# Kernel tuning notes

Measured on AMD Instinct MI355X. Metric: run time of the kernel, lower is better.

The kernel has to match this reference:

```python
import jax, jax.numpy as jnp
import numpy as np

B, I, A_IN = 32, 32, 16     # batch, input capsules, input atoms
OD, OA = 10, 16             # output_dim (classes), output_atoms
H, W = 12, 12               # spatial grid
NUM_ROUTING = 3


def _squash(t):
    # squash over atom dim (axis=2): x/|x| * |x|^2/(1+|x|^2) = x*|x|/(1+|x|^2)
    norm = jnp.linalg.norm(t, axis=2, keepdims=True)
    return t * norm / (1.0 + norm * norm)


def setup_inputs() -> dict:
    key = jax.random.key(0)
    k1, k2 = jax.random.split(key)
    x = jax.random.normal(k1, (B, I, A_IN, H, W), dtype=jnp.float32)
    # torch weight: (I, A_IN, OD*OA, 1, 1), init N(0, 0.1)
    weight = 0.1 * jax.random.normal(k2, (I, A_IN, OD * OA), dtype=jnp.float32)
    # torch bias: (OD, OA, 1, 1), init const 0.1
    bias = jnp.full((OD, OA, 1, 1), 0.1, dtype=jnp.float32)
    return {"x": x, "weight": weight, "bias": bias}


def reference(x, weight, bias):
    # votes: sum over input atoms -> [B, I, OD*OA, H, W] -> [B, I, OD, OA, H, W]
    votes = jnp.einsum("biahw,iak->bikhw", x, weight)
    votes = votes.reshape(B, I, OD, OA, H, W)
    biases = jnp.broadcast_to(bias, (OD, OA, H, W))

    # Dynamic routing. In the original, logits carry no gradient (built from
    # .data), so intermediate iterations are fully stop-gradient.
    votes_sg = jax.lax.stop_gradient(votes)
    logits = jnp.zeros((B, I, OD, H, W), dtype=votes.dtype)
    activation = None
    for i in range(NUM_ROUTING):
        route = jax.nn.softmax(logits, axis=2)  # softmax over output_dim
        v = votes if i == NUM_ROUTING - 1 else votes_sg
        preact = jnp.einsum("bidhw,bidahw->bdahw", route, v) + biases
        activation = _squash(preact)  # [B, OD, OA, H, W]
        if i < NUM_ROUTING - 1:
            # agreement (dot over atoms) updates logits
            logits = logits + jnp.einsum(
                "bidahw,bdahw->bidhw", votes_sg, jax.lax.stop_gradient(activation)
            )
    return activation
```

## Files before the change

kernel.cpp:

```cpp
#include <hip/hip_runtime.h>
#include <math.h>

#define NB 32
#define NI 32
#define NA 16
#define NOD 10
#define NOA 16
#define NK 160
#define NHW 144
#define NROUT 3
#define NROWS (NB*NHW)
#define SVLD 168

__device__ __forceinline__ unsigned short f2bf(float f) {
    unsigned b = __builtin_bit_cast(unsigned, f);
    b += 0x7fffu + ((b >> 16) & 1u);
    return (unsigned short)(b >> 16);
}
__device__ __forceinline__ float bf_lo(unsigned d) {
    return __builtin_bit_cast(float, d << 16);
}
__device__ __forceinline__ float bf_hi(unsigned d) {
    return __builtin_bit_cast(float, d & 0xffff0000u);
}

__global__ __launch_bounds__(256)
void capsule_fused_kernel(const float* __restrict__ x,
                          const float* __restrict__ weight,
                          const float* __restrict__ bias,
                          float* __restrict__ out)
{
    __shared__ unsigned short sv[4][NI][SVLD];
    __shared__ __align__(16) float pool[2048];
    float* const srt_f  = pool;
    float* const sact_f = pool + 4 * NOD * 33;

    const int tid  = threadIdx.x;
    const int w    = tid >> 6;
    const int l    = tid & 63;
    const int b    = blockIdx.x / (NHW / 4);
    const int hw0  = (blockIdx.x % (NHW / 4)) * 4;

    {
        const float* xb = x + ((size_t)b * NI * NA) * NHW + hw0;
        for (int j = tid; j < NI * NA; j += 256) {
            const float4 v = *reinterpret_cast<const float4*>(xb + (size_t)j * NHW);
            *reinterpret_cast<float4*>(&pool[j * 4]) = v;
        }
    }
    __syncthreads();

    for (int j = tid; j < NI * 40; j += 256) {
        const int i  = j / 40;
        const int kq = j - i * 40;
        const int k0 = kq * 4;
        const float4* wp = reinterpret_cast<const float4*>(
            weight + (size_t)i * NA * NK + k0);
        float4 a0 = make_float4(0.f, 0.f, 0.f, 0.f);
        float4 a1 = make_float4(0.f, 0.f, 0.f, 0.f);
        float4 a2 = make_float4(0.f, 0.f, 0.f, 0.f);
        float4 a3 = make_float4(0.f, 0.f, 0.f, 0.f);
#pragma unroll
        for (int a = 0; a < NA; ++a) {
            const float4 w4 = wp[(size_t)a * 40];
            const float4 xa = *reinterpret_cast<const float4*>(&pool[(i * NA + a) * 4]);
            a0.x = fmaf(xa.x, w4.x, a0.x); a0.y = fmaf(xa.x, w4.y, a0.y);
            a0.z = fmaf(xa.x, w4.z, a0.z); a0.w = fmaf(xa.x, w4.w, a0.w);
            a1.x = fmaf(xa.y, w4.x, a1.x); a1.y = fmaf(xa.y, w4.y, a1.y);
            a1.z = fmaf(xa.y, w4.z, a1.z); a1.w = fmaf(xa.y, w4.w, a1.w);
            a2.x = fmaf(xa.z, w4.x, a2.x); a2.y = fmaf(xa.z, w4.y, a2.y);
            a2.z = fmaf(xa.z, w4.z, a2.z); a2.w = fmaf(xa.z, w4.w, a2.w);
            a3.x = fmaf(xa.w, w4.x, a3.x); a3.y = fmaf(xa.w, w4.y, a3.y);
            a3.z = fmaf(xa.w, w4.z, a3.z); a3.w = fmaf(xa.w, w4.w, a3.w);
        }
        *reinterpret_cast<ushort4*>(&sv[0][i][k0]) =
            make_ushort4(f2bf(a0.x), f2bf(a0.y), f2bf(a0.z), f2bf(a0.w));
        *reinterpret_cast<ushort4*>(&sv[1][i][k0]) =
            make_ushort4(f2bf(a1.x), f2bf(a1.y), f2bf(a1.z), f2bf(a1.w));
        *reinterpret_cast<ushort4*>(&sv[2][i][k0]) =
            make_ushort4(f2bf(a2.x), f2bf(a2.y), f2bf(a2.z), f2bf(a2.w));
        *reinterpret_cast<ushort4*>(&sv[3][i][k0]) =
            make_ushort4(f2bf(a3.x), f2bf(a3.y), f2bf(a3.z), f2bf(a3.w));
    }

    const float2 b0 = *reinterpret_cast<const float2*>(bias + 2 * l);
    float2 b1 = make_float2(0.f, 0.f);
    if (l < 16) b1 = *reinterpret_cast<const float2*>(bias + 128 + 2 * l);

    float lg[NOD];
#pragma unroll
    for (int od = 0; od < NOD; ++od) lg[od] = 0.f;
    const int iown = l & 31;

    __syncthreads();

    for (int it = 0; it < NROUT; ++it) {
        {
            float m = lg[0];
#pragma unroll
            for (int od = 1; od < NOD; ++od) m = fmaxf(m, lg[od]);
            float e[NOD];
            float s = 0.f;
#pragma unroll
            for (int od = 0; od < NOD; ++od) {
                e[od] = __expf(lg[od] - m);
                s += e[od];
            }
            const float inv = 1.f / s;
            if (l < 32) {
#pragma unroll
                for (int od = 0; od < NOD; ++od)
                    srt_f[(w * NOD + od) * 33 + iown] = e[od] * inv;
            }
        }
        __builtin_amdgcn_wave_barrier();

        {
            const int od0 = l >> 3;
            float a0 = b0.x, a1 = b0.y;
#pragma unroll
            for (int i = 0; i < NI; ++i) {
                const unsigned d = *reinterpret_cast<const unsigned*>(&sv[w][i][2 * l]);
                const float r = srt_f[(w * NOD + od0) * 33 + i];
                a0 = fmaf(r, bf_lo(d), a0);
                a1 = fmaf(r, bf_hi(d), a1);
            }
            float ss = a0 * a0 + a1 * a1;
            ss += __shfl_xor(ss, 1, 8);
            ss += __shfl_xor(ss, 2, 8);
            ss += __shfl_xor(ss, 4, 8);
            const float sc = sqrtf(ss) / (1.f + ss);
            *reinterpret_cast<float2*>(&sact_f[w * 164 + 2 * l]) =
                make_float2(a0 * sc, a1 * sc);

            if (l < 16) {
                const int od1 = 8 + (l >> 3);
                float c0 = b1.x, c1 = b1.y;
#pragma unroll
                for (int i = 0; i < NI; ++i) {
                    const unsigned d = *reinterpret_cast<const unsigned*>(&sv[w][i][128 + 2 * l]);
                    const float r = srt_f[(w * NOD + od1) * 33 + i];
                    c0 = fmaf(r, bf_lo(d), c0);
                    c1 = fmaf(r, bf_hi(d), c1);
                }
                float s2 = c0 * c0 + c1 * c1;
                s2 += __shfl_xor(s2, 1, 8);
                s2 += __shfl_xor(s2, 2, 8);
                s2 += __shfl_xor(s2, 4, 8);
                const float sc2 = sqrtf(s2) / (1.f + s2);
                *reinterpret_cast<float2*>(&sact_f[w * 164 + 128 + 2 * l]) =
                    make_float2(c0 * sc2, c1 * sc2);
            }
        }
        __builtin_amdgcn_wave_barrier();

        if (it < NROUT - 1) {
#pragma unroll
            for (int r = 0; r < 5; ++r) {
                const int t  = l + 64 * r;
                const int i  = t & 31;
                const int od = t >> 5;
                const uint4 d0 = *reinterpret_cast<const uint4*>(&sv[w][i][od * NOA]);
                const uint4 d1 = *reinterpret_cast<const uint4*>(&sv[w][i][od * NOA + 8]);
                const float* ap = &sact_f[w * 164 + od * NOA];
                const float4 c0 = *reinterpret_cast<const float4*>(ap + 0);
                const float4 c1 = *reinterpret_cast<const float4*>(ap + 4);
                const float4 c2 = *reinterpret_cast<const float4*>(ap + 8);
                const float4 c3 = *reinterpret_cast<const float4*>(ap + 12);
                float acc;
                acc  = bf_lo(d0.x) * c0.x;
                acc = fmaf(bf_hi(d0.x), c0.y, acc);
                acc = fmaf(bf_lo(d0.y), c0.z, acc);
                acc = fmaf(bf_hi(d0.y), c0.w, acc);
                acc = fmaf(bf_lo(d0.z), c1.x, acc);
                acc = fmaf(bf_hi(d0.z), c1.y, acc);
                acc = fmaf(bf_lo(d0.w), c1.z, acc);
                acc = fmaf(bf_hi(d0.w), c1.w, acc);
                acc = fmaf(bf_lo(d1.x), c2.x, acc);
                acc = fmaf(bf_hi(d1.x), c2.y, acc);
                acc = fmaf(bf_lo(d1.y), c2.z, acc);
                acc = fmaf(bf_hi(d1.y), c2.w, acc);
                acc = fmaf(bf_lo(d1.z), c3.x, acc);
                acc = fmaf(bf_hi(d1.z), c3.y, acc);
                acc = fmaf(bf_lo(d1.w), c3.z, acc);
                acc = fmaf(bf_hi(d1.w), c3.w, acc);
                srt_f[(w * NOD + od) * 33 + i] = acc;
            }
            __builtin_amdgcn_wave_barrier();
#pragma unroll
            for (int od = 0; od < NOD; ++od)
                lg[od] += srt_f[(w * NOD + od) * 33 + iown];
            __builtin_amdgcn_wave_barrier();
        }
    }

    __syncthreads();
    if (tid < NK) {
        const float4 v = make_float4(sact_f[0 * 164 + tid], sact_f[1 * 164 + tid],
                                     sact_f[2 * 164 + tid], sact_f[3 * 164 + tid]);
        *reinterpret_cast<float4*>(out + ((size_t)b * NK + tid) * NHW + hw0) = v;
    }
}

extern "C" void kernel_launch(void* const* d_in, const int* in_sizes, int n_in,
                              void* d_out, int out_size, void* d_ws, size_t ws_size,
                              hipStream_t stream) {
    const float* x      = (const float*)d_in[0];
    const float* weight = (const float*)d_in[1];
    const float* bias   = (const float*)d_in[2];
    float* out          = (float*)d_out;

    capsule_fused_kernel<<<NROWS / 4, 256, 0, stream>>>(x, weight, bias, out);
}
```

Measured before the change: 43.54 us.

## Add prepass converting weights to bf16 and transposing x for coalesced loads

Adds a prepass kernel that converts the weight tensor to bf16 and transposes x so each block's 4-pixel slab is contiguous. The main kernel then copies x with fully contiguous float4 loads and reads weights as packed bf16 uint4, halving weight traffic and changing the per-thread tiling to 8 outputs. This removes strided 16-byte gathers of x and fp32 weight reads, at the cost of an extra kernel launch, a round trip of x through workspace, and bf16 rounding of the weights. The original kernel remains as a fallback when the workspace is too small.

```diff
diff --git a/kernel.cpp b/kernel.cpp
--- a/kernel.cpp
+++ b/kernel.cpp
@@ -12,6 +12,9 @@
 #define NROWS (NB*NHW)
 #define SVLD 168
 
+#define XT_OFF 262144
+#define WS_NEEDED (XT_OFF + (size_t)NROWS * 512 * 4)
+
 __device__ __forceinline__ unsigned short f2bf(float f) {
     unsigned b = __builtin_bit_cast(unsigned, f);
     b += 0x7fffu + ((b >> 16) & 1u);
@@ -25,62 +28,115 @@
 }
 
 __global__ __launch_bounds__(256)
-void capsule_fused_kernel(const float* __restrict__ x,
-                          const float* __restrict__ weight,
-                          const float* __restrict__ bias,
-                          float* __restrict__ out)
+void prepass_kernel(const float* __restrict__ x,
+                    const float* __restrict__ weight,
+                    unsigned short* __restrict__ w_bf,
+                    float* __restrict__ x_t)
+{
+    int bid = blockIdx.x;
+    const int tid = threadIdx.x;
+    if (bid < 320) {
+        const int idx = bid * 256 + tid;
+        w_bf[idx] = f2bf(weight[idx]);
+        return;
+    }
+    bid -= 320;
+    const int b  = bid / 72;
+    const int r  = bid % 72;
+    const int jt = r / 9;
+    const int ht = r % 9;
+    const int j0 = jt * 64, hw0 = ht * 16;
+
+    __shared__ float tile[64][17];
+    {
+        const int hh = tid & 15;
+        const int j1 = tid >> 4;
+#pragma unroll
+        for (int s = 0; s < 4; ++s) {
+            const int jj = j1 + s * 16;
+            tile[jj][hh] = x[(size_t)b * 73728 + (size_t)(j0 + jj) * NHW + hw0 + hh];
+        }
+    }
+    __syncthreads();
+    {
+        const int jj = tid >> 2;
+        const int p  = tid & 3;
+#pragma unroll
+        for (int s = 0; s < 4; ++s) {
+            const int hwg = ht * 4 + s;
+            x_t[((size_t)b * 36 + hwg) * 2048 + (size_t)(j0 + jj) * 4 + p] =
+                tile[jj][s * 4 + p];
+        }
+    }
+}
+
+__global__ __launch_bounds__(256)
+void capsule_fused2_kernel(const float* __restrict__ x_t,
+                           const unsigned short* __restrict__ w_bf,
+                           const float* __restrict__ bias,
+                           float* __restrict__ out)
 {
     __shared__ unsigned short sv[4][NI][SVLD];
     __shared__ __align__(16) float pool[2048];
     float* const srt_f  = pool;
     float* const sact_f = pool + 4 * NOD * 33;
 
-    const int tid  = threadIdx.x;
-    const int w    = tid >> 6;
-    const int l    = tid & 63;
-    const int b    = blockIdx.x / (NHW / 4);
-    const int hw0  = (blockIdx.x % (NHW / 4)) * 4;
+    const int tid = threadIdx.x;
+    const int w   = tid >> 6;
+    const int l   = tid & 63;
+    const int b   = blockIdx.x / (NHW / 4);
+    const int hw0 = (blockIdx.x % (NHW / 4)) * 4;
 
     {
-        const float* xb = x + ((size_t)b * NI * NA) * NHW + hw0;
-        for (int j = tid; j < NI * NA; j += 256) {
-            const float4 v = *reinterpret_cast<const float4*>(xb + (size_t)j * NHW);
-            *reinterpret_cast<float4*>(&pool[j * 4]) = v;
-        }
-    }
-    __syncthreads();
-
-    for (int j = tid; j < NI * 40; j += 256) {
-        const int i  = j / 40;
-        const int kq = j - i * 40;
-        const int k0 = kq * 4;
-        const float4* wp = reinterpret_cast<const float4*>(
-            weight + (size_t)i * NA * NK + k0);
-        float4 a0 = make_float4(0.f, 0.f, 0.f, 0.f);
-        float4 a1 = make_float4(0.f, 0.f, 0.f, 0.f);
-        float4 a2 = make_float4(0.f, 0.f, 0.f, 0.f);
-        float4 a3 = make_float4(0.f, 0.f, 0.f, 0.f);
+        const float4* src = reinterpret_cast<const float4*>(x_t + (size_t)blockIdx.x * 2048);
+        float4* dst = reinterpret_cast<float4*>(pool);
+        dst[tid]       = src[tid];
+        dst[tid + 256] = src[tid + 256];
+    }
+    __syncthreads();
+
+    for (int t = tid; t < NI * 20; t += 256) {
+        const int i  = t / 20;
+        const int ko = t - i * 20;
+        const int k0 = ko * 8;
+        const uint4* wp = reinterpret_cast<const uint4*>(w_bf + (size_t)i * NA * NK + k0);
+        float4 acc[4][2];
+#pragma unroll
+        for (int p = 0; p < 4; ++p) {
+            acc[p][0] = make_float4(0.f, 0.f, 0.f, 0.f);
+            acc[p][1] = make_float4(0.f, 0.f, 0.f, 0.f);
+        }
 #pragma unroll
         for (int a = 0; a < NA; ++a) {
-            const float4 w4 = wp[(size_t)a * 40];
+            const uint4 wv = wp[(size_t)a * 20];
+            const float w0 = bf_lo(wv.x), w1 = bf_hi(wv.x);
+            const float w2 = bf_lo(wv.y), w3 = bf_hi(wv.y);
+            const float w4 = bf_lo(wv.z), w5 = bf_hi(wv.z);
+            const float w6 = bf_lo(wv.w), w7 = bf_hi(wv.w);
             const float4 xa = *reinterpret_cast<const float4*>(&pool[(i * NA + a) * 4]);
-            a0.x = fmaf(xa.x, w4.x, a0.x); a0.y = fmaf(xa.x, w4.y, a0.y);
-            a0.z = fmaf(xa.x, w4.z, a0.z); a0.w = fmaf(xa.x, w4.w, a0.w);
-            a1.x = fmaf(xa.y, w4.x, a1.x); a1.y = fmaf(xa.y, w4.y, a1.y);
-            a1.z = fmaf(xa.y, w4.z, a1.z); a1.w = fmaf(xa.y, w4.w, a1.w);
-            a2.x = fmaf(xa.z, w4.x, a2.x); a2.y = fmaf(xa.z, w4.y, a2.y);
-            a2.z = fmaf(xa.z, w4.z, a2.z); a2.w = fmaf(xa.z, w4.w, a2.w);
-            a3.x = fmaf(xa.w, w4.x, a3.x); a3.y = fmaf(xa.w, w4.y, a3.y);
-            a3.z = fmaf(xa.w, w4.z, a3.z); a3.w = fmaf(xa.w, w4.w, a3.w);
-        }
-        *reinterpret_cast<ushort4*>(&sv[0][i][k0]) =
-            make_ushort4(f2bf(a0.x), f2bf(a0.y), f2bf(a0.z), f2bf(a0.w));
-        *reinterpret_cast<ushort4*>(&sv[1][i][k0]) =
-            make_ushort4(f2bf(a1.x), f2bf(a1.y), f2bf(a1.z), f2bf(a1.w));
-        *reinterpret_cast<ushort4*>(&sv[2][i][k0]) =
-            make_ushort4(f2bf(a2.x), f2bf(a2.y), f2bf(a2.z), f2bf(a2.w));
-        *reinterpret_cast<ushort4*>(&sv[3][i][k0]) =
-            make_ushort4(f2bf(a3.x), f2bf(a3.y), f2bf(a3.z), f2bf(a3.w));
+            const float xs[4] = {xa.x, xa.y, xa.z, xa.w};
+#pragma unroll
+            for (int p = 0; p < 4; ++p) {
+                const float xv = xs[p];
+                acc[p][0].x = fmaf(xv, w0, acc[p][0].x);
+                acc[p][0].y = fmaf(xv, w1, acc[p][0].y);
+                acc[p][0].z = fmaf(xv, w2, acc[p][0].z);
+                acc[p][0].w = fmaf(xv, w3, acc[p][0].w);
+                acc[p][1].x = fmaf(xv, w4, acc[p][1].x);
+                acc[p][1].y = fmaf(xv, w5, acc[p][1].y);
+                acc[p][1].z = fmaf(xv, w6, acc[p][1].z);
+                acc[p][1].w = fmaf(xv, w7, acc[p][1].w);
+            }
+        }
+#pragma unroll
+        for (int p = 0; p < 4; ++p) {
+            *reinterpret_cast<ushort4*>(&sv[p][i][k0]) =
+                make_ushort4(f2bf(acc[p][0].x), f2bf(acc[p][0].y),
+                             f2bf(acc[p][0].z), f2bf(acc[p][0].w));
+            *reinterpret_cast<ushort4*>(&sv[p][i][k0 + 4]) =
+                make_ushort4(f2bf(acc[p][1].x), f2bf(acc[p][1].y),
+                             f2bf(acc[p][1].z), f2bf(acc[p][1].w));
+        }
     }
 
     const float2 b0 = *reinterpret_cast<const float2*>(bias + 2 * l);
@@ -202,6 +258,173 @@
     }
 }
 
+__global__ __launch_bounds__(256)
+void capsule_fused_kernel(const float* __restrict__ x,
+                          const float* __restrict__ weight,
+                          const float* __restrict__ bias,
+                          float* __restrict__ out)
+{
+    __shared__ unsigned short sv[4][NI][SVLD];
+    __shared__ __align__(16) float pool[2048];
+    float* const srt_f  = pool;
+    float* const sact_f = pool + 4 * NOD * 33;
+
+    const int tid = threadIdx.x;
+    const int w   = tid >> 6;
+    const int l   = tid & 63;
+    const int b   = blockIdx.x / (NHW / 4);
+    const int hw0 = (blockIdx.x % (NHW / 4)) * 4;
+
+    {
+        const float* xb = x + ((size_t)b * NI * NA) * NHW + hw0;
+        for (int j = tid; j < NI * NA; j += 256) {
+            const float4 v = *reinterpret_cast<const float4*>(xb + (size_t)j * NHW);
+            *reinterpret_cast<float4*>(&pool[j * 4]) = v;
+        }
+    }
+    __syncthreads();
+
+    for (int j = tid; j < NI * 40; j += 256) {
+        const int i  = j / 40;
+        const int kq = j - i * 40;
+        const int k0 = kq * 4;
+        const float4* wp = reinterpret_cast<const float4*>(weight + (size_t)i * NA * NK + k0);
+        float4 a0 = make_float4(0.f,0.f,0.f,0.f), a1 = a0, a2 = a0, a3 = a0;
+#pragma unroll
+        for (int a = 0; a < NA; ++a) {
+            const float4 w4 = wp[(size_t)a * 40];
+            const float4 xa = *reinterpret_cast<const float4*>(&pool[(i * NA + a) * 4]);
+            a0.x = fmaf(xa.x, w4.x, a0.x); a0.y = fmaf(xa.x, w4.y, a0.y);
+            a0.z = fmaf(xa.x, w4.z, a0.z); a0.w = fmaf(xa.x, w4.w, a0.w);
+            a1.x = fmaf(xa.y, w4.x, a1.x); a1.y = fmaf(xa.y, w4.y, a1.y);
+            a1.z = fmaf(xa.y, w4.z, a1.z); a1.w = fmaf(xa.y, w4.w, a1.w);
+            a2.x = fmaf(xa.z, w4.x, a2.x); a2.y = fmaf(xa.z, w4.y, a2.y);
+            a2.z = fmaf(xa.z, w4.z, a2.z); a2.w = fmaf(xa.z, w4.w, a2.w);
+            a3.x = fmaf(xa.w, w4.x, a3.x); a3.y = fmaf(xa.w, w4.y, a3.y);
+            a3.z = fmaf(xa.w, w4.z, a3.z); a3.w = fmaf(xa.w, w4.w, a3.w);
+        }
+        *reinterpret_cast<ushort4*>(&sv[0][i][k0]) =
+            make_ushort4(f2bf(a0.x), f2bf(a0.y), f2bf(a0.z), f2bf(a0.w));
+        *reinterpret_cast<ushort4*>(&sv[1][i][k0]) =
+            make_ushort4(f2bf(a1.x), f2bf(a1.y), f2bf(a1.z), f2bf(a1.w));
+        *reinterpret_cast<ushort4*>(&sv[2][i][k0]) =
+            make_ushort4(f2bf(a2.x), f2bf(a2.y), f2bf(a2.z), f2bf(a2.w));
+        *reinterpret_cast<ushort4*>(&sv[3][i][k0]) =
+            make_ushort4(f2bf(a3.x), f2bf(a3.y), f2bf(a3.z), f2bf(a3.w));
+    }
+
+    const float2 b0 = *reinterpret_cast<const float2*>(bias + 2 * l);
+    float2 b1 = make_float2(0.f, 0.f);
+    if (l < 16) b1 = *reinterpret_cast<const float2*>(bias + 128 + 2 * l);
+
+    float lg[NOD];
+#pragma unroll
+    for (int od = 0; od < NOD; ++od) lg[od] = 0.f;
+    const int iown = l & 31;
+
+    __syncthreads();
+
+    for (int it = 0; it < NROUT; ++it) {
+        {
+            float m = lg[0];
+#pragma unroll
+            for (int od = 1; od < NOD; ++od) m = fmaxf(m, lg[od]);
+            float e[NOD];
+            float s = 0.f;
+#pragma unroll
+            for (int od = 0; od < NOD; ++od) { e[od] = __expf(lg[od] - m); s += e[od]; }
+            const float inv = 1.f / s;
+            if (l < 32) {
+#pragma unroll
+                for (int od = 0; od < NOD; ++od)
+                    srt_f[(w * NOD + od) * 33 + iown] = e[od] * inv;
+            }
+        }
+        __builtin_amdgcn_wave_barrier();
+        {
+            const int od0 = l >> 3;
+            float a0 = b0.x, a1 = b0.y;
+#pragma unroll
+            for (int i = 0; i < NI; ++i) {
+                const unsigned d = *reinterpret_cast<const unsigned*>(&sv[w][i][2 * l]);
+                const float r = srt_f[(w * NOD + od0) * 33 + i];
+                a0 = fmaf(r, bf_lo(d), a0);
+                a1 = fmaf(r, bf_hi(d), a1);
+            }
+            float ss = a0 * a0 + a1 * a1;
+            ss += __shfl_xor(ss, 1, 8);
+            ss += __shfl_xor(ss, 2, 8);
+            ss += __shfl_xor(ss, 4, 8);
+            const float sc = sqrtf(ss) / (1.f + ss);
+            *reinterpret_cast<float2*>(&sact_f[w * 164 + 2 * l]) = make_float2(a0 * sc, a1 * sc);
+            if (l < 16) {
+                const int od1 = 8 + (l >> 3);
+                float c0 = b1.x, c1 = b1.y;
+#pragma unroll
+                for (int i = 0; i < NI; ++i) {
+                    const unsigned d = *reinterpret_cast<const unsigned*>(&sv[w][i][128 + 2 * l]);
+                    const float r = srt_f[(w * NOD + od1) * 33 + i];
+                    c0 = fmaf(r, bf_lo(d), c0);
+                    c1 = fmaf(r, bf_hi(d), c1);
+                }
+                float s2 = c0 * c0 + c1 * c1;
+                s2 += __shfl_xor(s2, 1, 8);
+                s2 += __shfl_xor(s2, 2, 8);
+                s2 += __shfl_xor(s2, 4, 8);
+                const float sc2 = sqrtf(s2) / (1.f + s2);
+                *reinterpret_cast<float2*>(&sact_f[w * 164 + 128 + 2 * l]) =
+                    make_float2(c0 * sc2, c1 * sc2);
+            }
+        }
+        __builtin_amdgcn_wave_barrier();
+        if (it < NROUT - 1) {
+#pragma unroll
+            for (int r = 0; r < 5; ++r) {
+                const int t  = l + 64 * r;
+                const int i  = t & 31;
+                const int od = t >> 5;
+                const uint4 d0 = *reinterpret_cast<const uint4*>(&sv[w][i][od * NOA]);
+                const uint4 d1 = *reinterpret_cast<const uint4*>(&sv[w][i][od * NOA + 8]);
+                const float* ap = &sact_f[w * 164 + od * NOA];
+                const float4 c0 = *reinterpret_cast<const float4*>(ap + 0);
+                const float4 c1 = *reinterpret_cast<const float4*>(ap + 4);
+                const float4 c2 = *reinterpret_cast<const float4*>(ap + 8);
+                const float4 c3 = *reinterpret_cast<const float4*>(ap + 12);
+                float acc;
+                acc  = bf_lo(d0.x) * c0.x;
+                acc = fmaf(bf_hi(d0.x), c0.y, acc);
+                acc = fmaf(bf_lo(d0.y), c0.z, acc);
+                acc = fmaf(bf_hi(d0.y), c0.w, acc);
+                acc = fmaf(bf_lo(d0.z), c1.x, acc);
+                acc = fmaf(bf_hi(d0.z), c1.y, acc);
+                acc = fmaf(bf_lo(d0.w), c1.z, acc);
+                acc = fmaf(bf_hi(d0.w), c1.w, acc);
+                acc = fmaf(bf_lo(d1.x), c2.x, acc);
+                acc = fmaf(bf_hi(d1.x), c2.y, acc);
+                acc = fmaf(bf_lo(d1.y), c2.z, acc);
+                acc = fmaf(bf_hi(d1.y), c2.w, acc);
+                acc = fmaf(bf_lo(d1.z), c3.x, acc);
+                acc = fmaf(bf_hi(d1.z), c3.y, acc);
+                acc = fmaf(bf_lo(d1.w), c3.z, acc);
+                acc = fmaf(bf_hi(d1.w), c3.w, acc);
+                srt_f[(w * NOD + od) * 33 + i] = acc;
+            }
+            __builtin_amdgcn_wave_barrier();
+#pragma unroll
+            for (int od = 0; od < NOD; ++od)
+                lg[od] += srt_f[(w * NOD + od) * 33 + iown];
+            __builtin_amdgcn_wave_barrier();
+        }
+    }
+
+    __syncthreads();
+    if (tid < NK) {
+        const float4 v = make_float4(sact_f[0 * 164 + tid], sact_f[1 * 164 + tid],
+                                     sact_f[2 * 164 + tid], sact_f[3 * 164 + tid]);
+        *reinterpret_cast<float4*>(out + ((size_t)b * NK + tid) * NHW + hw0) = v;
+    }
+}
+
 extern "C" void kernel_launch(void* const* d_in, const int* in_sizes, int n_in,
                               void* d_out, int out_size, void* d_ws, size_t ws_size,
                               hipStream_t stream) {
@@ -210,5 +433,12 @@
     const float* bias   = (const float*)d_in[2];
     float* out          = (float*)d_out;
 
-    capsule_fused_kernel<<<NROWS / 4, 256, 0, stream>>>(x, weight, bias, out);
-}
+    if (ws_size >= WS_NEEDED) {
+        unsigned short* w_bf = (unsigned short*)d_ws;
+        float* x_t = (float*)((char*)d_ws + XT_OFF);
+        prepass_kernel<<<320 + NB * 72, 256, 0, stream>>>(x, weight, w_bf, x_t);
+        capsule_fused2_kernel<<<NROWS / 4, 256, 0, stream>>>(x_t, w_bf, bias, out);
+    } else {
+        capsule_fused_kernel<<<NROWS / 4, 256, 0, stream>>>(x, weight, bias, out);
+    }
+}
```

After: 47.98 us. 10.2% more time.

## Split each routing column across two waves with bf16 shared logits

Applied to the files above, without the earlier changes.

Doubles the block to 512 threads so two waves share each spatial column, each owning half of the output classes. Routing logits now live in double-buffered bf16 shared memory with block barriers between iterations, replacing per-thread registers. The weighted-sum step is recast so each lane covers 4 atoms over 16 inputs, with a pair-shuffle to combine halves. The first iteration uses the constant uniform route. The vote projection is retiled across 512 threads. The aim is more parallelism per column and shorter serial chains, at the cost of __syncthreads, bf16 rounding of logits and routes, and higher register pressure under launch_bounds(512,4).

```diff
diff --git a/kernel.cpp b/kernel.cpp
--- a/kernel.cpp
+++ b/kernel.cpp
@@ -17,6 +17,9 @@
     b += 0x7fffu + ((b >> 16) & 1u);
     return (unsigned short)(b >> 16);
 }
+__device__ __forceinline__ float bf2f(unsigned short u) {
+    return __builtin_bit_cast(float, (unsigned)u << 16);
+}
 __device__ __forceinline__ float bf_lo(unsigned d) {
     return __builtin_bit_cast(float, d << 16);
 }
@@ -24,173 +27,190 @@
     return __builtin_bit_cast(float, d & 0xffff0000u);
 }
 
-__global__ __launch_bounds__(256)
-void capsule_fused_kernel(const float* __restrict__ x,
-                          const float* __restrict__ weight,
-                          const float* __restrict__ bias,
-                          float* __restrict__ out)
+__global__ __launch_bounds__(512, 4)
+void capsule_fused7_kernel(const float* __restrict__ x,
+                           const float* __restrict__ weight,
+                           const float* __restrict__ bias,
+                           float* __restrict__ out)
 {
     __shared__ unsigned short sv[4][NI][SVLD];
-    __shared__ __align__(16) float pool[2048];
-    float* const srt_f  = pool;
-    float* const sact_f = pool + 4 * NOD * 33;
-
-    const int tid  = threadIdx.x;
-    const int w    = tid >> 6;
-    const int l    = tid & 63;
-    const int b    = blockIdx.x / (NHW / 4);
-    const int hw0  = (blockIdx.x % (NHW / 4)) * 4;
+    __shared__ __align__(16) float smem[2696];
+    unsigned short* const slog_h = (unsigned short*)smem;
+    unsigned short* const srt_h  = (unsigned short*)(smem + 1360);
+    float* const sact_f          = smem + 2040;
+    float* const xp              = smem;
+
+    const int tid = threadIdx.x;
+    const int wid = tid >> 6;
+    const int l   = tid & 63;
+    const int w2  = wid >> 1;
+    const int hf  = wid & 1;
+    const int b   = blockIdx.x / (NHW / 4);
+    const int hw0 = (blockIdx.x % (NHW / 4)) * 4;
 
     {
-        const float* xb = x + ((size_t)b * NI * NA) * NHW + hw0;
-        for (int j = tid; j < NI * NA; j += 256) {
-            const float4 v = *reinterpret_cast<const float4*>(xb + (size_t)j * NHW);
-            *reinterpret_cast<float4*>(&pool[j * 4]) = v;
-        }
+        const float4 v = *reinterpret_cast<const float4*>(
+            x + ((size_t)b * NI * NA + tid) * NHW + hw0);
+        *reinterpret_cast<float4*>(&xp[tid * 4]) = v;
     }
     __syncthreads();
 
-    for (int j = tid; j < NI * 40; j += 256) {
-        const int i  = j / 40;
-        const int kq = j - i * 40;
-        const int k0 = kq * 4;
-        const float4* wp = reinterpret_cast<const float4*>(
-            weight + (size_t)i * NA * NK + k0);
-        float4 a0 = make_float4(0.f, 0.f, 0.f, 0.f);
-        float4 a1 = make_float4(0.f, 0.f, 0.f, 0.f);
-        float4 a2 = make_float4(0.f, 0.f, 0.f, 0.f);
-        float4 a3 = make_float4(0.f, 0.f, 0.f, 0.f);
+    {
+        const int i  = tid >> 4;
+        const int tk = tid & 15;
+        const float* wb = weight + (size_t)i * NA * NK + 2 * tk;
+        float acc[5][4][2];
+#pragma unroll
+        for (int j = 0; j < 5; ++j)
+#pragma unroll
+            for (int r = 0; r < 4; ++r) { acc[j][r][0] = 0.f; acc[j][r][1] = 0.f; }
+
 #pragma unroll
         for (int a = 0; a < NA; ++a) {
-            const float4 w4 = wp[(size_t)a * 40];
-            const float4 xa = *reinterpret_cast<const float4*>(&pool[(i * NA + a) * 4]);
-            a0.x = fmaf(xa.x, w4.x, a0.x); a0.y = fmaf(xa.x, w4.y, a0.y);
-            a0.z = fmaf(xa.x, w4.z, a0.z); a0.w = fmaf(xa.x, w4.w, a0.w);
-            a1.x = fmaf(xa.y, w4.x, a1.x); a1.y = fmaf(xa.y, w4.y, a1.y);
-            a1.z = fmaf(xa.y, w4.z, a1.z); a1.w = fmaf(xa.y, w4.w, a1.w);
-            a2.x = fmaf(xa.z, w4.x, a2.x); a2.y = fmaf(xa.z, w4.y, a2.y);
-            a2.z = fmaf(xa.z, w4.z, a2.z); a2.w = fmaf(xa.z, w4.w, a2.w);
-            a3.x = fmaf(xa.w, w4.x, a3.x); a3.y = fmaf(xa.w, w4.y, a3.y);
-            a3.z = fmaf(xa.w, w4.z, a3.z); a3.w = fmaf(xa.w, w4.w, a3.w);
-        }
-        *reinterpret_cast<ushort4*>(&sv[0][i][k0]) =
-            make_ushort4(f2bf(a0.x), f2bf(a0.y), f2bf(a0.z), f2bf(a0.w));
-        *reinterpret_cast<ushort4*>(&sv[1][i][k0]) =
-            make_ushort4(f2bf(a1.x), f2bf(a1.y), f2bf(a1.z), f2bf(a1.w));
-        *reinterpret_cast<ushort4*>(&sv[2][i][k0]) =
-            make_ushort4(f2bf(a2.x), f2bf(a2.y), f2bf(a2.z), f2bf(a2.w));
-        *reinterpret_cast<ushort4*>(&sv[3][i][k0]) =
-            make_ushort4(f2bf(a3.x), f2bf(a3.y), f2bf(a3.z), f2bf(a3.w));
-    }
-
-    const float2 b0 = *reinterpret_cast<const float2*>(bias + 2 * l);
-    float2 b1 = make_float2(0.f, 0.f);
-    if (l < 16) b1 = *reinterpret_cast<const float2*>(bias + 128 + 2 * l);
-
-    float lg[NOD];
-#pragma unroll
-    for (int od = 0; od < NOD; ++od) lg[od] = 0.f;
-    const int iown = l & 31;
+            const float4 xa = *reinterpret_cast<const float4*>(&xp[(i * NA + a) * 4]);
+            const float xr[4] = {xa.x, xa.y, xa.z, xa.w};
+#pragma unroll
+            for (int j = 0; j < 5; ++j) {
+                const float2 w2v = *reinterpret_cast<const float2*>(
+                    wb + (size_t)a * NK + 32 * j);
+#pragma unroll
+                for (int r = 0; r < 4; ++r) {
+                    acc[j][r][0] = fmaf(xr[r], w2v.x, acc[j][r][0]);
+                    acc[j][r][1] = fmaf(xr[r], w2v.y, acc[j][r][1]);
+                }
+            }
+        }
+#pragma unroll
+        for (int j = 0; j < 5; ++j) {
+            const int k0 = 2 * tk + 32 * j;
+#pragma unroll
+            for (int r = 0; r < 4; ++r) {
+                const ushort2 s = make_ushort2(f2bf(acc[j][r][0]), f2bf(acc[j][r][1]));
+                *reinterpret_cast<ushort2*>(&sv[r][i][k0]) = s;
+            }
+        }
+    }
+
+    const int kb = hf * 80;
+    const int ob = hf * 5;
+    int hh = 0, odg = 0, kg = 0;
+    float4 bq = make_float4(0.f, 0.f, 0.f, 0.f);
+    if (l < 40) {
+        const int kq = l >> 1;
+        hh  = l & 1;
+        odg = ob + (kq >> 2);
+        kg  = kb + kq * 4;
+        if (hh == 0)
+            bq = *reinterpret_cast<const float4*>(bias + kg);
+    }
+    const int li = l & 31;
+
+    float lgp[3] = {0.f, 0.f, 0.f};
 
     __syncthreads();
 
     for (int it = 0; it < NROUT; ++it) {
-        {
-            float m = lg[0];
-#pragma unroll
-            for (int od = 1; od < NOD; ++od) m = fmaxf(m, lg[od]);
+        if (it > 0) {
+            const int rbuf = it & 1;
             float e[NOD];
+            float m = -1e30f;
+#pragma unroll
+            for (int od = 0; od < NOD; ++od) {
+                e[od] = bf2f(slog_h[((rbuf * 4 + w2) * NOD + od) * 34 + li]);
+                m = fmaxf(m, e[od]);
+            }
             float s = 0.f;
 #pragma unroll
             for (int od = 0; od < NOD; ++od) {
-                e[od] = __expf(lg[od] - m);
+                e[od] = __expf(e[od] - m);
                 s += e[od];
             }
             const float inv = 1.f / s;
             if (l < 32) {
 #pragma unroll
-                for (int od = 0; od < NOD; ++od)
-                    srt_f[(w * NOD + od) * 33 + iown] = e[od] * inv;
-            }
-        }
-        __builtin_amdgcn_wave_barrier();
-
-        {
-            const int od0 = l >> 3;
-            float a0 = b0.x, a1 = b0.y;
-#pragma unroll
-            for (int i = 0; i < NI; ++i) {
-                const unsigned d = *reinterpret_cast<const unsigned*>(&sv[w][i][2 * l]);
-                const float r = srt_f[(w * NOD + od0) * 33 + i];
-                a0 = fmaf(r, bf_lo(d), a0);
-                a1 = fmaf(r, bf_hi(d), a1);
-            }
-            float ss = a0 * a0 + a1 * a1;
-            ss += __shfl_xor(ss, 1, 8);
+                for (int odl = 0; odl < 5; ++odl)
+                    srt_h[((w2 * NOD) + ob + odl) * 34 + li] = f2bf(e[ob + odl] * inv);
+            }
+            __builtin_amdgcn_wave_barrier();
+        }
+
+        if (l < 40) {
+            float a0 = bq.x, a1 = bq.y, a2 = bq.z, a3 = bq.w;
+            const unsigned short* svb  = &sv[w2][hh * 16][kg];
+            const unsigned short* srow = &srt_h[(w2 * NOD + odg) * 34 + hh * 16];
+#pragma unroll
+            for (int s2 = 0; s2 < 8; ++s2) {
+                float r0, r1;
+                if (it == 0) {
+                    r0 = 0.1f; r1 = 0.1f;
+                } else {
+                    const unsigned u = *reinterpret_cast<const unsigned*>(srow + 2 * s2);
+                    r0 = bf_lo(u); r1 = bf_hi(u);
+                }
+                const uint2 d0 = *reinterpret_cast<const uint2*>(svb + (2 * s2) * SVLD);
+                const uint2 d1 = *reinterpret_cast<const uint2*>(svb + (2 * s2 + 1) * SVLD);
+                a0 = fmaf(r0, bf_lo(d0.x), a0);
+                a1 = fmaf(r0, bf_hi(d0.x), a1);
+                a2 = fmaf(r0, bf_lo(d0.y), a2);
+                a3 = fmaf(r0, bf_hi(d0.y), a3);
+                a0 = fmaf(r1, bf_lo(d1.x), a0);
+                a1 = fmaf(r1, bf_hi(d1.x), a1);
+                a2 = fmaf(r1, bf_lo(d1.y), a2);
+                a3 = fmaf(r1, bf_hi(d1.y), a3);
+            }
+            a0 += __shfl_xor(a0, 1, 2);
+            a1 += __shfl_xor(a1, 1, 2);
+            a2 += __shfl_xor(a2, 1, 2);
+            a3 += __shfl_xor(a3, 1, 2);
+            float ss = a0 * a0 + a1 * a1 + a2 * a2 + a3 * a3;
             ss += __shfl_xor(ss, 2, 8);
             ss += __shfl_xor(ss, 4, 8);
             const float sc = sqrtf(ss) / (1.f + ss);
-            *reinterpret_cast<float2*>(&sact_f[w * 164 + 2 * l]) =
-                make_float2(a0 * sc, a1 * sc);
-
-            if (l < 16) {
-                const int od1 = 8 + (l >> 3);
-                float c0 = b1.x, c1 = b1.y;
-#pragma unroll
-                for (int i = 0; i < NI; ++i) {
-                    const unsigned d = *reinterpret_cast<const unsigned*>(&sv[w][i][128 + 2 * l]);
-                    const float r = srt_f[(w * NOD + od1) * 33 + i];
-                    c0 = fmaf(r, bf_lo(d), c0);
-                    c1 = fmaf(r, bf_hi(d), c1);
+            if (hh == 0)
+                *reinterpret_cast<float4*>(&sact_f[w2 * 164 + kg]) =
+                    make_float4(a0 * sc, a1 * sc, a2 * sc, a3 * sc);
+        }
+        __builtin_amdgcn_wave_barrier();
+
+        if (it < NROUT - 1) {
+            const int wbuf = (it + 1) & 1;
+#pragma unroll
+            for (int r = 0; r < 3; ++r) {
+                const int t = l + 64 * r;
+                if (t < 160) {
+                    const int odl = t >> 5;
+                    const int i   = t & 31;
+                    const int od  = ob + odl;
+                    const int kk  = od * 16;
+                    const uint4 d0 = *reinterpret_cast<const uint4*>(&sv[w2][i][kk]);
+                    const uint4 d1 = *reinterpret_cast<const uint4*>(&sv[w2][i][kk + 8]);
+                    const float* ap = &sact_f[w2 * 164 + kk];
+                    const float4 c0 = *reinterpret_cast<const float4*>(ap + 0);
+                    const float4 c1 = *reinterpret_cast<const float4*>(ap + 4);
+                    const float4 c2 = *reinterpret_cast<const float4*>(ap + 8);
+                    const float4 c3 = *reinterpret_cast<const float4*>(ap + 12);
+                    float acc;
+                    acc  = bf_lo(d0.x) * c0.x;
+                    acc = fmaf(bf_hi(d0.x), c0.y, acc);
+                    acc = fmaf(bf_lo(d0.y), c0.z, acc);
+                    acc = fmaf(bf_hi(d0.y), c0.w, acc);
+                    acc = fmaf(bf_lo(d0.z), c1.x, acc);
+                    acc = fmaf(bf_hi(d0.z), c1.y, acc);
+                    acc = fmaf(bf_lo(d0.w), c1.z, acc);
+                    acc = fmaf(bf_hi(d0.w), c1.w, acc);
+                    acc = fmaf(bf_lo(d1.x), c2.x, acc);
+                    acc = fmaf(bf_hi(d1.x), c2.y, acc);
+                    acc = fmaf(bf_lo(d1.y), c2.z, acc);
+                    acc = fmaf(bf_hi(d1.y), c2.w, acc);
+                    acc = fmaf(bf_lo(d1.z), c3.x, acc);
+                    acc = fmaf(bf_hi(d1.z), c3.y, acc);
+                    acc = fmaf(bf_lo(d1.w), c3.z, acc);
+                    acc = fmaf(bf_hi(d1.w), c3.w, acc);
+                    lgp[r] += acc;
+                    slog_h[((wbuf * 4 + w2) * NOD + od) * 34 + i] = f2bf(lgp[r]);
                 }
-                float s2 = c0 * c0 + c1 * c1;
-                s2 += __shfl_xor(s2, 1, 8);
-                s2 += __shfl_xor(s2, 2, 8);
-                s2 += __shfl_xor(s2, 4, 8);
-                const float sc2 = sqrtf(s2) / (1.f + s2);
-                *reinterpret_cast<float2*>(&sact_f[w * 164 + 128 + 2 * l]) =
-                    make_float2(c0 * sc2, c1 * sc2);
-            }
-        }
-        __builtin_amdgcn_wave_barrier();
-
-        if (it < NROUT - 1) {
-#pragma unroll
-            for (int r = 0; r < 5; ++r) {
-                const int t  = l + 64 * r;
-                const int i  = t & 31;
-                const int od = t >> 5;
-                const uint4 d0 = *reinterpret_cast<const uint4*>(&sv[w][i][od * NOA]);
-                const uint4 d1 = *reinterpret_cast<const uint4*>(&sv[w][i][od * NOA + 8]);
-                const float* ap = &sact_f[w * 164 + od * NOA];
-                const float4 c0 = *reinterpret_cast<const float4*>(ap + 0);
-                const float4 c1 = *reinterpret_cast<const float4*>(ap + 4);
-                const float4 c2 = *reinterpret_cast<const float4*>(ap + 8);
-                const float4 c3 = *reinterpret_cast<const float4*>(ap + 12);
-                float acc;
-                acc  = bf_lo(d0.x) * c0.x;
-                acc = fmaf(bf_hi(d0.x), c0.y, acc);
-                acc = fmaf(bf_lo(d0.y), c0.z, acc);
-                acc = fmaf(bf_hi(d0.y), c0.w, acc);
-                acc = fmaf(bf_lo(d0.z), c1.x, acc);
-                acc = fmaf(bf_hi(d0.z), c1.y, acc);
-                acc = fmaf(bf_lo(d0.w), c1.z, acc);
-                acc = fmaf(bf_hi(d0.w), c1.w, acc);
-                acc = fmaf(bf_lo(d1.x), c2.x, acc);
-                acc = fmaf(bf_hi(d1.x), c2.y, acc);
-                acc = fmaf(bf_lo(d1.y), c2.z, acc);
-                acc = fmaf(bf_hi(d1.y), c2.w, acc);
-                acc = fmaf(bf_lo(d1.z), c3.x, acc);
-                acc = fmaf(bf_hi(d1.z), c3.y, acc);
-                acc = fmaf(bf_lo(d1.w), c3.z, acc);
-                acc = fmaf(bf_hi(d1.w), c3.w, acc);
-                srt_f[(w * NOD + od) * 33 + i] = acc;
-            }
-            __builtin_amdgcn_wave_barrier();
-#pragma unroll
-            for (int od = 0; od < NOD; ++od)
-                lg[od] += srt_f[(w * NOD + od) * 33 + iown];
-            __builtin_amdgcn_wave_barrier();
+            }
+            __syncthreads();
         }
     }
 
@@ -210,5 +230,5 @@
     const float* bias   = (const float*)d_in[2];
     float* out          = (float*)d_out;
 
-    capsule_fused_kernel<<<NROWS / 4, 256, 0, stream>>>(x, weight, bias, out);
-}
+    capsule_fused7_kernel<<<NROWS / 4, 512, 0, stream>>>(x, weight, bias, out);
+}
```

New measurement: 49.31 us. 13.2% more time.
